# Kernel optimization log

Measured on AMD Instinct MI355X. Metric: run time of the kernel, lower is better.

The kernel has to match this reference:

```python
import jax, jax.numpy as jnp
import numpy as np

WL_IDX = 0          # water_level_index
THRESH = 0.1        # anomaly threshold
B, T, I, H, O = 2048, 2048, 8, 24, 1


def setup_inputs() -> dict:
    key = jax.random.key(0)
    ks = jax.random.split(key, 7)
    s = float(1.0 / np.sqrt(H))  # PyTorch LSTMCell/Linear uniform init bound
    x = jax.random.normal(ks[0], (B, T, I), dtype=jnp.float32)
    W_ih = jax.random.uniform(ks[1], (4 * H, I), minval=-s, maxval=s, dtype=jnp.float32)
    W_hh = jax.random.uniform(ks[2], (4 * H, H), minval=-s, maxval=s, dtype=jnp.float32)
    b_ih = jax.random.uniform(ks[3], (4 * H,), minval=-s, maxval=s, dtype=jnp.float32)
    b_hh = jax.random.uniform(ks[4], (4 * H,), minval=-s, maxval=s, dtype=jnp.float32)
    W_out = jax.random.uniform(ks[5], (O, H), minval=-s, maxval=s, dtype=jnp.float32)
    b_out = jax.random.uniform(ks[6], (O,), minval=-s, maxval=s, dtype=jnp.float32)
    return {"x": x, "W_ih": W_ih, "W_hh": W_hh, "b_ih": b_ih, "b_hh": b_hh,
            "W_out": W_out, "b_out": b_out}


def reference(x, W_ih, W_hh, b_ih, b_hh, W_out, b_out):
    # x: (B, T, I) -> preds: (B, T, O)
    Bs, Ts, Is = x.shape
    Hs = W_hh.shape[1]
    h0 = jnp.zeros((Bs, Hs), x.dtype)
    c0 = jnp.zeros((Bs, Hs), x.dtype)
    # Init pred equal to t=0 water level -> anomaly flag is False at t=0,
    # reproducing the original's ungated first step.
    pred0 = x[:, 0, WL_IDX:WL_IDX + 1]  # (B, 1)
    xs = jnp.swapaxes(x, 0, 1)  # (T, B, I)

    def step(carry, x_t):
        h, c, pred = carry
        actual = x_t[:, WL_IDX:WL_IDX + 1]            # (B, 1)
        anom = jnp.abs(pred - actual) > THRESH         # (B, 1) bool
        wl = jnp.where(anom[:, 0], pred[:, 0], x_t[:, WL_IDX])
        inp = x_t.at[:, WL_IDX].set(wl)                # anomaly-gated input
        # LSTMCell: gates in PyTorch order i, f, g, o
        gates = inp @ W_ih.T + b_ih + h @ W_hh.T + b_hh  # (B, 4H)
        i_g, f_g, g_g, o_g = jnp.split(gates, 4, axis=1)
        c_new = jax.nn.sigmoid(f_g) * c + jax.nn.sigmoid(i_g) * jnp.tanh(g_g)
        h_new = jax.nn.sigmoid(o_g) * jnp.tanh(c_new)
        pred_new = h_new @ W_out.T + b_out             # (B, O)
        return (h_new, c_new, pred_new), pred_new

    _, preds = jax.lax.scan(step, (h0, c0, pred0), xs)  # (T, B, O)
    return jnp.swapaxes(preds, 0, 1)  # (B, T, O)
```

## Files before the change

kernel.cpp:

```cpp
#include <hip/hip_runtime.h>

#define TT 2048
#define II 8
#define HH 24
#define THRESH 0.1f
#define LOG2E 1.4426950408889634f

typedef float v4f __attribute__((ext_vector_type(4)));

#define ROR_ADD(a, N)                                                          \
    {                                                                          \
        int t_ = __builtin_amdgcn_update_dpp(0, __float_as_int(a),             \
                                             0x120 + (N), 0xF, 0xF, false);    \
        (a) += __int_as_float(t_);                                             \
    }

__global__ __launch_bounds__(64)
__attribute__((amdgpu_waves_per_eu(2, 2)))
void lstm_anom_kernel(const float* __restrict__ x,
                      const float* __restrict__ W_ih,
                      const float* __restrict__ W_hh,
                      const float* __restrict__ b_ih,
                      const float* __restrict__ b_hh,
                      const float* __restrict__ W_out,
                      const float* __restrict__ b_out,
                      float* __restrict__ out)
{
    __shared__ __align__(16) float vbuf[32];

    const int  lane  = threadIdx.x;
    const int  b     = blockIdx.x;
    const int  l32   = lane & 31;
    const bool hi    = lane >= 32;
    const bool unitL = (l32 < HH);
    const int  jc    = unitL ? l32 : 0;
    const bool xL    = (!hi) && (l32 >= 24);
    const int  xk    = l32 - 24;

    const float* xb = x + (size_t)b * (TT * II);

    const int rowA = (hi ? 2 * HH : 0) + jc;
    const int rowB = rowA + HH;
    v4f wA4[8], wB4[8];
    wA4[0] = *(const v4f*)(W_ih + rowA * II);
    wA4[1] = *(const v4f*)(W_ih + rowA * II + 4);
    wB4[0] = *(const v4f*)(W_ih + rowB * II);
    wB4[1] = *(const v4f*)(W_ih + rowB * II + 4);
    #pragma unroll
    for (int q = 0; q < 6; ++q) {
        wA4[2 + q] = *(const v4f*)(W_hh + rowA * HH + q * 4);
        wB4[2 + q] = *(const v4f*)(W_hh + rowB * HH + q * 4);
    }
    const float biasA = b_ih[rowA] + b_hh[rowA];
    const float biasB = b_ih[rowB] + b_hh[rowB];
    const float kA = hi ? (-2.f * LOG2E) : (-LOG2E);
    const float mA = hi ? 2.f : 1.f;
    const float nA = hi ? -1.f : 0.f;
    const float woutj = unitL ? W_out[jc] : 0.f;
    const float bout  = b_out[0];

    if (lane < 32) vbuf[lane] = (lane < 8) ? xb[lane] : 0.f;
    float xA = 0.f, xB = 0.f;
    if (xL) xA = xb[II + xk];
    __syncthreads();

    const v4f* pv = (const v4f*)vbuf;
    v4f vv[8];
    #pragma unroll
    for (int q = 0; q < 8; ++q) vv[q] = pv[q];

    float pred = vv[0].x;
    float cst = 0.f, predsave = 0.f;

    for (int t = 0; t < TT; ++t) {
        vv[0].x = (fabsf(pred - vv[0].x) > THRESH) ? pred : vv[0].x;

        v4f accA = (v4f){biasA, 0.f, 0.f, 0.f};
        v4f accB = (v4f){biasB, 0.f, 0.f, 0.f};
        #pragma unroll
        for (int q = 0; q < 8; ++q) {
            accA = __builtin_elementwise_fma(wA4[q], vv[q], accA);
            accB = __builtin_elementwise_fma(wB4[q], vv[q], accB);
        }
        const float aA = (accA.x + accA.y) + (accA.z + accA.w);
        const float aB = (accB.x + accB.y) + (accB.z + accB.w);

        const float sA = __builtin_amdgcn_rcpf(1.f + __builtin_amdgcn_exp2f(kA * aA));
        const float tA = fmaf(sA, mA, nA);
        const float sB = __builtin_amdgcn_rcpf(1.f + __builtin_amdgcn_exp2f(-LOG2E * aB));
        auto rA = __builtin_amdgcn_permlane32_swap(__float_as_int(tA), __float_as_int(tA), false, false);
        auto rB = __builtin_amdgcn_permlane32_swap(__float_as_int(sB), __float_as_int(sB), false, false);
        const float ig = __int_as_float(rA[0]);
        const float gg = __int_as_float(rA[1]);
        const float fg = __int_as_float(rB[0]);
        const float og = __int_as_float(rB[1]);

        cst = fmaf(fg, cst, ig * gg);
        const float sc = __builtin_amdgcn_rcpf(1.f + __builtin_amdgcn_exp2f(-2.f * LOG2E * cst));
        const float tc = fmaf(2.f, sc, -1.f);
        const float h  = og * tc;

        if (lane < 32) vbuf[xL ? xk : (8 + l32)] = xL ? xA : h;
        if (xL) {
            int tn = t + 2; if (tn > TT - 1) tn = TT - 1;
            xB = xb[(size_t)tn * II + xk];
        }

        float p = woutj * h;
        {
            auto r = __builtin_amdgcn_permlane16_swap(__float_as_int(p), __float_as_int(p), false, false);
            p = __int_as_float(r[0]) + __int_as_float(r[1]);
        }
        ROR_ADD(p, 8); ROR_ADD(p, 4); ROR_ADD(p, 2); ROR_ADD(p, 1);
        pred = p + bout;

        predsave = ((t & 63) == lane) ? pred : predsave;
        if ((t & 63) == 63) out[(size_t)b * TT + (t - 63) + lane] = predsave;

        #pragma unroll
        for (int q = 0; q < 8; ++q) vv[q] = pv[q];
        if (xL) xA = xB;
    }
}

extern "C" void kernel_launch(void* const* d_in, const int* in_sizes, int n_in,
                              void* d_out, int out_size, void* d_ws, size_t ws_size,
                              hipStream_t stream) {
    const float* x     = (const float*)d_in[0];
    const float* W_ih  = (const float*)d_in[1];
    const float* W_hh  = (const float*)d_in[2];
    const float* b_ih  = (const float*)d_in[3];
    const float* b_hh  = (const float*)d_in[4];
    const float* W_out = (const float*)d_in[5];
    const float* b_out = (const float*)d_in[6];
    float* out = (float*)d_out;

    dim3 grid(2048);
    dim3 block(64);
    lstm_anom_kernel<<<grid, block, 0, stream>>>(x, W_ih, W_hh, b_ih, b_hh,
                                                 W_out, b_out, out);
}
```

Measured before the change: 777.6 us.

## Broadcast hidden state via readlane into SGPRs instead of LDS round-trip

Removes the per-step LDS write/read of the hidden state and input vector. The hidden state is broadcast with 24 v_readlane instructions into scalar registers, and each lane loads x[t+1] directly, prefetched one step ahead. The dot product becomes scalar FMAs with two accumulators per gate. This avoids LDS latency on the serial recurrence chain, at the cost of 24 readlanes per step, their VALU-to-SGPR dependency stalls, and longer FMA chains.

Result: slower. 927.4 us (+19.3%).

```diff
diff --git a/kernel.cpp b/kernel.cpp
--- a/kernel.cpp
+++ b/kernel.cpp
@@ -6,14 +6,16 @@
 #define THRESH 0.1f
 #define LOG2E 1.4426950408889634f
 
-typedef float v4f __attribute__((ext_vector_type(4)));
-
 #define ROR_ADD(a, N)                                                          \
     {                                                                          \
         int t_ = __builtin_amdgcn_update_dpp(0, __float_as_int(a),             \
                                              0x120 + (N), 0xF, 0xF, false);    \
         (a) += __int_as_float(t_);                                             \
     }
+
+__device__ __forceinline__ float readlane_f(float v, int l) {
+    return __int_as_float(__builtin_amdgcn_readlane(__float_as_int(v), l));
+}
 
 __global__ __launch_bounds__(64)
 __attribute__((amdgpu_waves_per_eu(2, 2)))
@@ -26,30 +28,31 @@
                       const float* __restrict__ b_out,
                       float* __restrict__ out)
 {
-    __shared__ __align__(16) float vbuf[32];
-
     const int  lane  = threadIdx.x;
     const int  b     = blockIdx.x;
     const int  l32   = lane & 31;
     const bool hi    = lane >= 32;
     const bool unitL = (l32 < HH);
     const int  jc    = unitL ? l32 : 0;
-    const bool xL    = (!hi) && (l32 >= 24);
-    const int  xk    = l32 - 24;
 
     const float* xb = x + (size_t)b * (TT * II);
 
     const int rowA = (hi ? 2 * HH : 0) + jc;
     const int rowB = rowA + HH;
-    v4f wA4[8], wB4[8];
-    wA4[0] = *(const v4f*)(W_ih + rowA * II);
-    wA4[1] = *(const v4f*)(W_ih + rowA * II + 4);
-    wB4[0] = *(const v4f*)(W_ih + rowB * II);
-    wB4[1] = *(const v4f*)(W_ih + rowB * II + 4);
+    float wA[32], wB[32];
+    #pragma unroll
+    for (int q = 0; q < 2; ++q) {
+        const float4 qa = *(const float4*)(W_ih + rowA * II + q * 4);
+        const float4 qb = *(const float4*)(W_ih + rowB * II + q * 4);
+        wA[q*4+0]=qa.x; wA[q*4+1]=qa.y; wA[q*4+2]=qa.z; wA[q*4+3]=qa.w;
+        wB[q*4+0]=qb.x; wB[q*4+1]=qb.y; wB[q*4+2]=qb.z; wB[q*4+3]=qb.w;
+    }
     #pragma unroll
     for (int q = 0; q < 6; ++q) {
-        wA4[2 + q] = *(const v4f*)(W_hh + rowA * HH + q * 4);
-        wB4[2 + q] = *(const v4f*)(W_hh + rowB * HH + q * 4);
+        const float4 qa = *(const float4*)(W_hh + rowA * HH + q * 4);
+        const float4 qb = *(const float4*)(W_hh + rowB * HH + q * 4);
+        wA[8+q*4+0]=qa.x; wA[8+q*4+1]=qa.y; wA[8+q*4+2]=qa.z; wA[8+q*4+3]=qa.w;
+        wB[8+q*4+0]=qb.x; wB[8+q*4+1]=qb.y; wB[8+q*4+2]=qb.z; wB[8+q*4+3]=qb.w;
     }
     const float biasA = b_ih[rowA] + b_hh[rowA];
     const float biasB = b_ih[rowB] + b_hh[rowB];
@@ -59,31 +62,40 @@
     const float woutj = unitL ? W_out[jc] : 0.f;
     const float bout  = b_out[0];
 
-    if (lane < 32) vbuf[lane] = (lane < 8) ? xb[lane] : 0.f;
-    float xA = 0.f, xB = 0.f;
-    if (xL) xA = xb[II + xk];
-    __syncthreads();
+    float cx[8], nx[8], sh[HH];
+    #pragma unroll
+    for (int k = 0; k < 8; ++k) cx[k] = xb[k];
+    #pragma unroll
+    for (int j = 0; j < HH; ++j) sh[j] = 0.f;
 
-    const v4f* pv = (const v4f*)vbuf;
-    v4f vv[8];
-    #pragma unroll
-    for (int q = 0; q < 8; ++q) vv[q] = pv[q];
-
-    float pred = vv[0].x;
+    float pred = cx[0];
     float cst = 0.f, predsave = 0.f;
 
     for (int t = 0; t < TT; ++t) {
-        vv[0].x = (fabsf(pred - vv[0].x) > THRESH) ? pred : vv[0].x;
+        const int tn = (t + 1 < TT) ? (t + 1) : (TT - 1);
+        #pragma unroll
+        for (int k = 0; k < 8; ++k) nx[k] = xb[(size_t)tn * II + k];
 
-        v4f accA = (v4f){biasA, 0.f, 0.f, 0.f};
-        v4f accB = (v4f){biasB, 0.f, 0.f, 0.f};
+        const float v0 = (fabsf(pred - cx[0]) > THRESH) ? pred : cx[0];
+
+        float aAx = fmaf(wA[0], v0, biasA), aAy = wA[1] * cx[1];
+        float aBx = fmaf(wB[0], v0, biasB), aBy = wB[1] * cx[1];
         #pragma unroll
-        for (int q = 0; q < 8; ++q) {
-            accA = __builtin_elementwise_fma(wA4[q], vv[q], accA);
-            accB = __builtin_elementwise_fma(wB4[q], vv[q], accB);
+        for (int k = 1; k < 4; ++k) {
+            aAx = fmaf(wA[2*k],   cx[2*k],   aAx);
+            aAy = fmaf(wA[2*k+1], cx[2*k+1], aAy);
+            aBx = fmaf(wB[2*k],   cx[2*k],   aBx);
+            aBy = fmaf(wB[2*k+1], cx[2*k+1], aBy);
         }
-        const float aA = (accA.x + accA.y) + (accA.z + accA.w);
-        const float aB = (accB.x + accB.y) + (accB.z + accB.w);
+        #pragma unroll
+        for (int k = 0; k < 12; ++k) {
+            aAx = fmaf(wA[8+2*k],   sh[2*k],   aAx);
+            aAy = fmaf(wA[8+2*k+1], sh[2*k+1], aAy);
+            aBx = fmaf(wB[8+2*k],   sh[2*k],   aBx);
+            aBy = fmaf(wB[8+2*k+1], sh[2*k+1], aBy);
+        }
+        const float aA = aAx + aAy;
+        const float aB = aBx + aBy;
 
         const float sA = __builtin_amdgcn_rcpf(1.f + __builtin_amdgcn_exp2f(kA * aA));
         const float tA = fmaf(sA, mA, nA);
@@ -100,11 +112,8 @@
         const float tc = fmaf(2.f, sc, -1.f);
         const float h  = og * tc;
 
-        if (lane < 32) vbuf[xL ? xk : (8 + l32)] = xL ? xA : h;
-        if (xL) {
-            int tn = t + 2; if (tn > TT - 1) tn = TT - 1;
-            xB = xb[(size_t)tn * II + xk];
-        }
+        #pragma unroll
+        for (int j = 0; j < HH; ++j) sh[j] = readlane_f(h, j);
 
         float p = woutj * h;
         {
@@ -118,8 +127,7 @@
         if ((t & 63) == 63) out[(size_t)b * TT + (t - 63) + lane] = predsave;
 
         #pragma unroll
-        for (int q = 0; q < 8; ++q) vv[q] = pv[q];
-        if (xL) xA = xB;
+        for (int k = 0; k < 8; ++k) cx[k] = nx[k];
     }
 }
 
```
